# Kernel tuning notes

Hardware: AMD Instinct MI355X
Metric: run time of the kernel (lower is better)

Reference implementation:

```python
import jax, jax.numpy as jnp
import numpy as np

EMBED_DIM = 512
NUM_HEADS = 8
HEAD_DIM = EMBED_DIM // NUM_HEADS  # 64
LN_EPS = 1e-5
SEQ = 2048
BATCH = 2


def sparsemax(z):
    """Sparsemax over last axis: euclidean projection of each row onto the simplex."""
    K = z.shape[-1]
    z_sorted = -jnp.sort(-z, axis=-1)                      # descending
    z_cumsum = jnp.cumsum(z_sorted, axis=-1)
    r = jnp.arange(1, K + 1, dtype=z.dtype)
    support = r * z_sorted > (z_cumsum - 1.0)
    k_int = jnp.sum(support.astype(jnp.int32), axis=-1, keepdims=True)  # support size >= 1
    tau_sum = jnp.take_along_axis(z_cumsum, k_int - 1, axis=-1)
    tau = (tau_sum - 1.0) / k_int.astype(z.dtype)
    return jnp.maximum(z - tau, 0.0)


def layer_norm(x, eps=LN_EPS):
    # per-head pattern normalization over head_dim, no affine (normalize_pattern_affine=False)
    mu = jnp.mean(x, axis=-1, keepdims=True)
    var = jnp.mean(jnp.square(x - mu), axis=-1, keepdims=True)
    return (x - mu) * jax.lax.rsqrt(var + eps)


def setup_inputs() -> dict:
    key = jax.random.key(0)
    ks = jax.random.split(key, 6)
    E = EMBED_DIM
    return {
        "query": jax.random.normal(ks[0], (SEQ, BATCH, E), dtype=jnp.float32),
        "key": jax.random.normal(ks[1], (SEQ, BATCH, E), dtype=jnp.float32),
        "value": jax.random.normal(ks[2], (SEQ, BATCH, E), dtype=jnp.float32),
        "in_proj_weight": 0.02 * jax.random.normal(ks[3], (3 * E, E), dtype=jnp.float32),
        "in_proj_bias": jnp.zeros((3 * E,), dtype=jnp.float32),
        "out_proj_weight": 0.02 * jax.random.normal(ks[4], (E, E), dtype=jnp.float32),
        "out_proj_bias": jnp.zeros((E,), dtype=jnp.float32),
        "update_steps_max": 0,  # single association pass
    }


def reference(query, key, value, in_proj_weight, in_proj_bias,
              out_proj_weight, out_proj_bias, update_steps_max):
    L, B, E = query.shape
    S = key.shape[0]
    H, D = NUM_HEADS, HEAD_DIM
    wq, wk, wv = in_proj_weight[:E], in_proj_weight[E:2 * E], in_proj_weight[2 * E:]
    bq, bk, bv = in_proj_bias[:E], in_proj_bias[E:2 * E], in_proj_bias[2 * E:]
    # projections (torch Linear: x @ W.T + b)
    q = (query @ wq.T + bq).reshape(L, B, H, D)
    k = (key @ wk.T + bk).reshape(S, B, H, D)
    v = (value @ wv.T + bv).reshape(S, B, H, D)
    # pattern normalization (normalize_pattern=True, no affine), then attention scaling
    q = layer_norm(q) * (float(D) ** -0.5)
    k = layer_norm(k)
    v = layer_norm(v)
    # association scores [B, H, Lq, Lk]
    scores = jnp.einsum('ibhd,jbhd->bhij', q, k)
    attn = sparsemax(scores)  # sparse='sparsemax' activation over key axis
    out = jnp.einsum('bhij,jbhd->ibhd', attn, v).reshape(L, B, E)
    return out @ out_proj_weight.T + out_proj_bias
```

## Files before the change

kernel.cpp:

```cpp
#include <hip/hip_runtime.h>

#define SEQ   2048
#define BATCH 2
#define EMB   512
#define NH    8

typedef short bf16x8 __attribute__((ext_vector_type(8)));
typedef float f32x4  __attribute__((ext_vector_type(4)));
typedef unsigned short u16;
typedef unsigned long long u64;

static __device__ __forceinline__ u16 f2bf(float f) {
    unsigned u = __float_as_uint(f);
    return (u16)((u + 0x7FFF + ((u >> 16) & 1)) >> 16);
}
static __device__ __forceinline__ float bf2f(u16 h) {
    return __uint_as_float((unsigned)h << 16);
}
static __device__ __forceinline__ unsigned cvtpk(float a, float b) {
    unsigned r;
    asm("v_cvt_pk_bf16_f32 %0, %1, %2" : "=v"(r) : "v"(a), "v"(b));
    return r;
}
static __device__ __forceinline__ void split8(const float* p, bf16x8& hi, bf16x8& lo) {
    const float4 f0 = *(const float4*)p;
    const float4 f1 = *(const float4*)(p + 4);
    const float fv[8] = {f0.x, f0.y, f0.z, f0.w, f1.x, f1.y, f1.z, f1.w};
    union { unsigned w[4]; bf16x8 v; } H, L;
#pragma unroll
    for (int q = 0; q < 4; ++q) {
        const float a = fv[2 * q], b = fv[2 * q + 1];
        const unsigned h = cvtpk(a, b);
        const float la = a - __uint_as_float(h << 16);
        const float lb = b - __uint_as_float(h & 0xFFFF0000u);
        H.w[q] = h;
        L.w[q] = cvtpk(la, lb);
    }
    hi = H.v; lo = L.v;
}

#define IW4 196608
#define W4  262144
__global__ __launch_bounds__(256) void convert_w(
    const float* __restrict__ ipw, const float* __restrict__ opw,
    u16* __restrict__ iwh, u16* __restrict__ iwl,
    u16* __restrict__ owh, u16* __restrict__ owl)
{
    const int f = blockIdx.x * 256 + threadIdx.x;
    if (f >= W4) return;
    const float* src; u16 *dh, *dl; int o;
    if (f < IW4) { src = ipw; dh = iwh; dl = iwl; o = f; }
    else         { src = opw; dh = owh; dl = owl; o = f - IW4; }
    const float4 x = ((const float4*)src)[o];
    ushort4 hi, lo;
    hi.x = f2bf(x.x); lo.x = f2bf(x.x - bf2f(hi.x));
    hi.y = f2bf(x.y); lo.y = f2bf(x.y - bf2f(hi.y));
    hi.z = f2bf(x.z); lo.z = f2bf(x.z - bf2f(hi.z));
    hi.w = f2bf(x.w); lo.w = f2bf(x.w - bf2f(hi.w));
    ((ushort4*)dh)[o] = hi;
    ((ushort4*)dl)[o] = lo;
}

__global__ __launch_bounds__(256, 4) void gemm_qkv_ln_mfma(
    const float* __restrict__ query, const float* __restrict__ key_in,
    const float* __restrict__ value,
    const u16* __restrict__ iwh, const u16* __restrict__ iwl,
    const float* __restrict__ ipb,
    u16* __restrict__ qhi, u16* __restrict__ qlo,
    u16* __restrict__ khi, u16* __restrict__ klo,
    u16* __restrict__ vth, u16* __restrict__ vtl)
{
    __shared__ float Et[8704];

    const int z = blockIdx.z;
    const float* Xf = (z == 0) ? query : (z == 1) ? key_in : value;
    const float scale = (z == 0) ? 0.125f : 1.0f;

    const int t0  = blockIdx.x * 128;
    const int h   = blockIdx.y;
    const int og0 = z * EMB + h * 64;

    const int tid = threadIdx.x;
    const int w   = tid >> 6;
    const int l   = tid & 63;
    const int c   = l & 15;
    const int g   = l >> 4;

    f32x4 acc[2][4];
#pragma unroll
    for (int mf = 0; mf < 2; ++mf)
#pragma unroll
        for (int nf = 0; nf < 4; ++nf) acc[mf][nf] = (f32x4){0.f, 0.f, 0.f, 0.f};

    const int arow0 = t0 + w * 32 + c;
#pragma unroll
    for (int ks = 0; ks < 16; ++ks) {
        const int k0 = ks * 32 + g * 8;
        bf16x8 ah[2], al[2], bh[4], bl[4];
#pragma unroll
        for (int mf = 0; mf < 2; ++mf)
            split8(&Xf[(size_t)(arow0 + mf * 16) * EMB + k0], ah[mf], al[mf]);
#pragma unroll
        for (int nf = 0; nf < 4; ++nf) {
            const size_t r = (size_t)(og0 + nf * 16 + c) * EMB + k0;
            bh[nf] = *(const bf16x8*)&iwh[r];
            bl[nf] = *(const bf16x8*)&iwl[r];
        }
#pragma unroll
        for (int mf = 0; mf < 2; ++mf)
#pragma unroll
            for (int nf = 0; nf < 4; ++nf) {
                f32x4 t = acc[mf][nf];
                t = __builtin_amdgcn_mfma_f32_16x16x32_bf16(ah[mf], bh[nf], t, 0, 0, 0);
                t = __builtin_amdgcn_mfma_f32_16x16x32_bf16(al[mf], bh[nf], t, 0, 0, 0);
                t = __builtin_amdgcn_mfma_f32_16x16x32_bf16(ah[mf], bl[nf], t, 0, 0, 0);
                acc[mf][nf] = t;
            }
    }

#pragma unroll
    for (int nf = 0; nf < 4; ++nf) {
        const float bj = ipb[og0 + nf * 16 + c];
#pragma unroll
        for (int mf = 0; mf < 2; ++mf)
#pragma unroll
            for (int j = 0; j < 4; ++j) acc[mf][nf][j] += bj;
    }

#pragma unroll
    for (int mf = 0; mf < 2; ++mf) {
        float mu[4], rs[4];
#pragma unroll
        for (int j = 0; j < 4; ++j) {
            float s = acc[mf][0][j] + acc[mf][1][j] + acc[mf][2][j] + acc[mf][3][j];
#pragma unroll
            for (int d = 1; d <= 8; d <<= 1) s += __shfl_xor(s, d);
            mu[j] = s * (1.0f / 64.0f);
        }
#pragma unroll
        for (int j = 0; j < 4; ++j) {
            float t = 0.f;
#pragma unroll
            for (int nf = 0; nf < 4; ++nf) {
                const float dv = acc[mf][nf][j] - mu[j];
                t += dv * dv;
            }
#pragma unroll
            for (int d = 1; d <= 8; d <<= 1) t += __shfl_xor(t, d);
            rs[j] = rsqrtf(t * (1.0f / 64.0f) + 1e-5f) * scale;
        }
#pragma unroll
        for (int j = 0; j < 4; ++j) {
            const int tl = w * 32 + mf * 16 + g * 4 + j;
#pragma unroll
            for (int nf = 0; nf < 4; ++nf) {
                const float val = (acc[mf][nf][j] - mu[j]) * rs[j];
                const int o = nf * 16 + c;
                if (z == 2) Et[o * 133 + tl] = val;
                else        Et[tl * 68 + o]  = val;
            }
        }
    }
    __syncthreads();

    const int part = tid & 7;
    if (z < 2) {
        u16* dh = (z == 0) ? qhi : khi;
        u16* dl = (z == 0) ? qlo : klo;
#pragma unroll
        for (int p = 0; p < 8; ++p) {
            const int seg = p * 32 + (tid >> 3);
            const int tl  = seg & 127;
            const int hl  = seg >> 7;
            const float4 v0 = *(const float4*)&Et[tl * 68 + part * 8];
            const float4 v1 = *(const float4*)&Et[tl * 68 + part * 8 + 4];
            const float vv[8] = {v0.x, v0.y, v0.z, v0.w, v1.x, v1.y, v1.z, v1.w};
            unsigned pk[4];
#pragma unroll
            for (int q = 0; q < 4; ++q) {
                u16 ua, ub;
                if (hl == 0) { ua = f2bf(vv[2*q]); ub = f2bf(vv[2*q+1]); }
                else {
                    const u16 ha = f2bf(vv[2*q]),  hb = f2bf(vv[2*q+1]);
                    ua = f2bf(vv[2*q] - bf2f(ha)); ub = f2bf(vv[2*q+1] - bf2f(hb));
                }
                pk[q] = (unsigned)ua | ((unsigned)ub << 16);
            }
            const int bh_ = (tl & 1) * NH + h;
            const int ii  = (t0 >> 1) + (tl >> 1);
            u16* dst = hl ? dl : dh;
            *(uint4*)&dst[((size_t)bh_ * SEQ + ii) * 64 + part * 8] =
                make_uint4(pk[0], pk[1], pk[2], pk[3]);
        }
    } else {
#pragma unroll
        for (int p = 0; p < 8; ++p) {
            const int seg  = p * 32 + (tid >> 3);
            const int d    = seg & 63;
            const int rest = seg >> 6;
            const int b    = rest & 1;
            const int hl   = rest >> 1;
            float vv[8];
#pragma unroll
            for (int k = 0; k < 8; ++k)
                vv[k] = Et[d * 133 + 2 * (part * 8 + k) + b];
            unsigned pk[4];
#pragma unroll
            for (int q = 0; q < 4; ++q) {
                u16 ua, ub;
                if (hl == 0) { ua = f2bf(vv[2*q]); ub = f2bf(vv[2*q+1]); }
                else {
                    const u16 ha = f2bf(vv[2*q]),  hb = f2bf(vv[2*q+1]);
                    ua = f2bf(vv[2*q] - bf2f(ha)); ub = f2bf(vv[2*q+1] - bf2f(hb));
                }
                pk[q] = (unsigned)ua | ((unsigned)ub << 16);
            }
            const int bh_ = b * NH + h;
            u16* dst = hl ? vtl : vth;
            *(uint4*)&dst[((size_t)bh_ * 64 + d) * SEQ + (t0 >> 1) + part * 8] =
                make_uint4(pk[0], pk[1], pk[2], pk[3]);
        }
    }
}

__global__ __launch_bounds__(512, 2) void attn_sparsemax_mfma(
    const u16* __restrict__ qhi, const u16* __restrict__ qlo,
    const u16* __restrict__ khi, const u16* __restrict__ klo,
    const u16* __restrict__ vth, const u16* __restrict__ vtl,
    u16* __restrict__ aoh, u16* __restrict__ aol)
{
    __shared__ float Opart[8][16][66];
    __shared__ u16   Pst[8][2][16][40];
    __shared__ float wred[2][8][32];
    __shared__ float wcnt[2][8][32];

    const int tid = threadIdx.x;
    const int w   = tid >> 6;
    const int l   = tid & 63;
    const int c   = l & 15;
    const int g   = l >> 4;

    const int wgid = blockIdx.x;
    const int xcd  = wgid & 7;
    const int idx  = wgid >> 3;
    const int bh   = xcd * 2 + (idx >> 6);
    const int q0   = (idx & 63) * 32;

    const size_t bhoff = (size_t)bh * SEQ * 64;
    const u16* qh  = qhi + bhoff;
    const u16* ql  = qlo + bhoff;
    const u16* kh  = khi + bhoff;
    const u16* kl  = klo + bhoff;
    const u16* vh_ = vth + bhoff;
    const u16* vl_ = vtl + bhoff;

    bf16x8 qhf[2][2], qlf[2][2];
#pragma unroll
    for (int nf = 0; nf < 2; ++nf)
#pragma unroll
        for (int kf = 0; kf < 2; ++kf) {
            const size_t a = (size_t)(q0 + nf * 16 + c) * 64 + kf * 32 + g * 8;
            qhf[nf][kf] = *(const bf16x8*)&qh[a];
            qlf[nf][kf] = *(const bf16x8*)&ql[a];
        }

    const int wbase = w * 256;
    f32x4 acc[16][2];
#pragma unroll
    for (int mf = 0; mf < 16; ++mf) {
        const size_t kr = (size_t)(wbase + mf * 16 + c) * 64 + g * 8;
        const bf16x8 kh0 = *(const bf16x8*)&kh[kr];
        const bf16x8 kh1 = *(const bf16x8*)&kh[kr + 32];
        const bf16x8 kl0 = *(const bf16x8*)&kl[kr];
        const bf16x8 kl1 = *(const bf16x8*)&kl[kr + 32];
#pragma unroll
        for (int nf = 0; nf < 2; ++nf) {
            f32x4 t = (f32x4){0.f, 0.f, 0.f, 0.f};
            t = __builtin_amdgcn_mfma_f32_16x16x32_bf16(kh0, qhf[nf][0], t, 0, 0, 0);
            t = __builtin_amdgcn_mfma_f32_16x16x32_bf16(kh1, qhf[nf][1], t, 0, 0, 0);
            t = __builtin_amdgcn_mfma_f32_16x16x32_bf16(kl0, qhf[nf][0], t, 0, 0, 0);
            t = __builtin_amdgcn_mfma_f32_16x16x32_bf16(kl1, qhf[nf][1], t, 0, 0, 0);
            t = __builtin_amdgcn_mfma_f32_16x16x32_bf16(kh0, qlf[nf][0], t, 0, 0, 0);
            t = __builtin_amdgcn_mfma_f32_16x16x32_bf16(kh1, qlf[nf][1], t, 0, 0, 0);
            acc[mf][nf] = t;
        }
    }

    {
        float mx[2];
#pragma unroll
        for (int nf = 0; nf < 2; ++nf) {
            float m = -1e30f;
#pragma unroll
            for (int mf = 0; mf < 16; ++mf)
#pragma unroll
                for (int r = 0; r < 4; ++r) m = fmaxf(m, acc[mf][nf][r]);
            m = fmaxf(m, __shfl_xor(m, 16));
            m = fmaxf(m, __shfl_xor(m, 32));
            mx[nf] = m;
        }
        if (g == 0) { wred[0][w][c] = mx[0]; wred[0][w][16 + c] = mx[1]; }
    }
    __syncthreads();

    float tau[2];
#pragma unroll
    for (int nf = 0; nf < 2; ++nf) {
        float m = -1e30f;
#pragma unroll
        for (int ww = 0; ww < 8; ++ww) m = fmaxf(m, wred[0][ww][nf * 16 + c]);
        tau[nf] = m - 1.0f;
    }

    int cprev[2] = {-1, -1};
    for (int it = 0; it < 24; ++it) {
        const int bs = (~it) & 1;
        float sj[2], cj[2];
#pragma unroll
        for (int nf = 0; nf < 2; ++nf) {
            float s = 0.f, cn = 0.f;
#pragma unroll
            for (int mf = 0; mf < 16; ++mf)
#pragma unroll
                for (int r = 0; r < 4; ++r) {
                    const float v = acc[mf][nf][r];
                    if (v > tau[nf]) { s += v; cn += 1.f; }
                }
            s  += __shfl_xor(s, 16);  cn += __shfl_xor(cn, 16);
            s  += __shfl_xor(s, 32);  cn += __shfl_xor(cn, 32);
            sj[nf] = s; cj[nf] = cn;
        }
        if (g == 0) {
            wred[bs][w][c]      = sj[0];  wred[bs][w][16 + c] = sj[1];
            wcnt[bs][w][c]      = cj[0];  wcnt[bs][w][16 + c] = cj[1];
        }
        __syncthreads();
        int changed = 0;
#pragma unroll
        for (int nf = 0; nf < 2; ++nf) {
            float S = 0.f, C = 0.f;
#pragma unroll
            for (int ww = 0; ww < 8; ++ww) {
                S += wred[bs][ww][nf * 16 + c];
                C += wcnt[bs][ww][nf * 16 + c];
            }
            tau[nf] = (S - 1.0f) / C;
            const int Ci = (int)C;
            changed |= (Ci != cprev[nf]);
            cprev[nf] = Ci;
        }
        if (!__any(changed)) break;
    }

    f32x4 Oacc[4][2];
#pragma unroll
    for (int mo = 0; mo < 4; ++mo)
#pragma unroll
        for (int nf = 0; nf < 2; ++nf) Oacc[mo][nf] = (f32x4){0.f, 0.f, 0.f, 0.f};

#pragma unroll
    for (int ks = 0; ks < 8; ++ks) {
        bf16x8 vh[4], vl[4];
#pragma unroll
        for (int mo = 0; mo < 4; ++mo) {
            const size_t va = (size_t)(mo * 16 + c) * SEQ + wbase + ks * 32 + g * 8;
            vh[mo] = *(const bf16x8*)&vh_[va];
            vl[mo] = *(const bf16x8*)&vl_[va];
        }
#pragma unroll
        for (int nf = 0; nf < 2; ++nf) {
#pragma unroll
            for (int m01 = 0; m01 < 2; ++m01) {
                const f32x4 s = acc[2 * ks + m01][nf];
                const float p0 = fmaxf(s[0] - tau[nf], 0.f);
                const float p1 = fmaxf(s[1] - tau[nf], 0.f);
                const float p2 = fmaxf(s[2] - tau[nf], 0.f);
                const float p3 = fmaxf(s[3] - tau[nf], 0.f);
                const unsigned h0 = cvtpk(p0, p1);
                const unsigned h1 = cvtpk(p2, p3);
                const unsigned l0 = cvtpk(p0 - __uint_as_float(h0 << 16),
                                          p1 - __uint_as_float(h0 & 0xFFFF0000u));
                const unsigned l1 = cvtpk(p2 - __uint_as_float(h1 << 16),
                                          p3 - __uint_as_float(h1 & 0xFFFF0000u));
                *(u64*)&Pst[w][0][c][m01 * 16 + g * 4] = (u64)h0 | ((u64)h1 << 32);
                *(u64*)&Pst[w][1][c][m01 * 16 + g * 4] = (u64)l0 | ((u64)l1 << 32);
            }
            const bf16x8 Bhi = *(const bf16x8*)&Pst[w][0][c][g * 8];
            const bf16x8 Blo = *(const bf16x8*)&Pst[w][1][c][g * 8];
#pragma unroll
            for (int mo = 0; mo < 4; ++mo) {
                f32x4 t = Oacc[mo][nf];
                t = __builtin_amdgcn_mfma_f32_16x16x32_bf16(vh[mo], Bhi, t, 0, 0, 0);
                t = __builtin_amdgcn_mfma_f32_16x16x32_bf16(vh[mo], Blo, t, 0, 0, 0);
                t = __builtin_amdgcn_mfma_f32_16x16x32_bf16(vl[mo], Bhi, t, 0, 0, 0);
                Oacc[mo][nf] = t;
            }
        }
    }

    const int b_ = bh >> 3, h_ = bh & 7;
#pragma unroll
    for (int nf = 0; nf < 2; ++nf) {
        if (nf) __syncthreads();
#pragma unroll
        for (int mo = 0; mo < 4; ++mo)
#pragma unroll
            for (int r = 0; r < 4; ++r)
                Opart[w][c][mo * 16 + 4 * g + r] = Oacc[mo][nf][r];
        __syncthreads();
#pragma unroll
        for (int p = 0; p < 2; ++p) {
            const int idx2 = p * 512 + tid;
            const int d = idx2 & 63;
            const int i = idx2 >> 6;
            float sv = 0.f;
#pragma unroll
            for (int ww = 0; ww < 8; ++ww) sv += Opart[ww][i][d];
            const int irow = q0 + nf * 16 + i;
            const size_t oa = (size_t)(irow * BATCH + b_) * EMB + h_ * 64 + d;
            const u16 hv = f2bf(sv);
            aoh[oa] = hv;
            aol[oa] = f2bf(sv - bf2f(hv));
        }
    }
}

__global__ __launch_bounds__(256, 4) void gemm_out_mfma(
    const u16* __restrict__ aoh, const u16* __restrict__ aol,
    const u16* __restrict__ owh, const u16* __restrict__ owl,
    const float* __restrict__ opb, float* __restrict__ out)
{
    __shared__ float Et[128 * 68];

    const int t0 = blockIdx.x * 128;
    const int o0 = blockIdx.y * 64;

    const int tid = threadIdx.x;
    const int w   = tid >> 6;
    const int l   = tid & 63;
    const int c   = l & 15;
    const int g   = l >> 4;

    f32x4 acc[2][4];
#pragma unroll
    for (int mf = 0; mf < 2; ++mf)
#pragma unroll
        for (int nf = 0; nf < 4; ++nf) acc[mf][nf] = (f32x4){0.f, 0.f, 0.f, 0.f};

    const int arow0 = t0 + w * 32 + c;
#pragma unroll
    for (int ks = 0; ks < 16; ++ks) {
        const int k0 = ks * 32 + g * 8;
        bf16x8 ah[2], al[2], bh[4], bl[4];
#pragma unroll
        for (int mf = 0; mf < 2; ++mf) {
            const size_t r = (size_t)(arow0 + mf * 16) * EMB + k0;
            ah[mf] = *(const bf16x8*)&aoh[r];
            al[mf] = *(const bf16x8*)&aol[r];
        }
#pragma unroll
        for (int nf = 0; nf < 4; ++nf) {
            const size_t r = (size_t)(o0 + nf * 16 + c) * EMB + k0;
            bh[nf] = *(const bf16x8*)&owh[r];
            bl[nf] = *(const bf16x8*)&owl[r];
        }
#pragma unroll
        for (int mf = 0; mf < 2; ++mf)
#pragma unroll
            for (int nf = 0; nf < 4; ++nf) {
                f32x4 t = acc[mf][nf];
                t = __builtin_amdgcn_mfma_f32_16x16x32_bf16(ah[mf], bh[nf], t, 0, 0, 0);
                t = __builtin_amdgcn_mfma_f32_16x16x32_bf16(al[mf], bh[nf], t, 0, 0, 0);
                t = __builtin_amdgcn_mfma_f32_16x16x32_bf16(ah[mf], bl[nf], t, 0, 0, 0);
                acc[mf][nf] = t;
            }
    }

#pragma unroll
    for (int mf = 0; mf < 2; ++mf)
#pragma unroll
        for (int j = 0; j < 4; ++j) {
            const int tl = w * 32 + mf * 16 + g * 4 + j;
#pragma unroll
            for (int nf = 0; nf < 4; ++nf)
                Et[tl * 68 + nf * 16 + c] = acc[mf][nf][j] + opb[o0 + nf * 16 + c];
        }
    __syncthreads();

    const int part = tid & 15;
#pragma unroll
    for (int p = 0; p < 8; ++p) {
        const int row = p * 16 + (tid >> 4);
        const float4 v = *(const float4*)&Et[row * 68 + part * 4];
        *(float4*)&out[(size_t)(t0 + row) * EMB + o0 + part * 4] = v;
    }
}

extern "C" void kernel_launch(void* const* d_in, const int* in_sizes, int n_in,
                              void* d_out, int out_size, void* d_ws, size_t ws_size,
                              hipStream_t stream)
{
    const float* query = (const float*)d_in[0];
    const float* key_  = (const float*)d_in[1];
    const float* value = (const float*)d_in[2];
    const float* ipw   = (const float*)d_in[3];
    const float* ipb   = (const float*)d_in[4];
    const float* opw   = (const float*)d_in[5];
    const float* opb   = (const float*)d_in[6];

    char* ws = (char*)d_ws;
    const size_t MB = 1024 * 1024;
    u16* qhi = (u16*)(ws + 0 * MB);
    u16* qlo = (u16*)(ws + 4 * MB);
    u16* khi = (u16*)(ws + 8 * MB);
    u16* klo = (u16*)(ws + 12 * MB);
    u16* vth = (u16*)(ws + 16 * MB);
    u16* vtl = (u16*)(ws + 20 * MB);
    u16* aoh = (u16*)(ws + 24 * MB);
    u16* aol = (u16*)(ws + 28 * MB);
    u16* iwh = (u16*)(ws + 32 * MB);
    u16* iwl = (u16*)(ws + 34 * MB);
    u16* owh = (u16*)(ws + 36 * MB);
    u16* owl = (u16*)(ws + 37 * MB);
    float* out = (float*)d_out;
    (void)ws_size; (void)in_sizes; (void)n_in; (void)out_size;

    convert_w<<<1024, 256, 0, stream>>>(ipw, opw, iwh, iwl, owh, owl);
    gemm_qkv_ln_mfma<<<dim3(32, 8, 3), 256, 0, stream>>>(
        query, key_, value, iwh, iwl, ipb, qhi, qlo, khi, klo, vth, vtl);
    attn_sparsemax_mfma<<<1024, 512, 0, stream>>>(
        qhi, qlo, khi, klo, vth, vtl, aoh, aol);
    gemm_out_mfma<<<dim3(32, 8), 256, 0, stream>>>(
        aoh, aol, owh, owl, opb, out);
}
```

Before: 369.2 us.

## Halve attention query tile to 16 rows and reduce partial outputs via LDS atomics

The attention kernel now processes 16 query rows per workgroup instead of 32, doubling the grid to 2048 blocks. Per-thread score and output accumulators drop by half, and launch bounds are raised to allow 4 workgroups per CU. The per-wave partial-output buffer and its serial 8-way reduction are replaced by a small zero-initialised LDS tile that waves accumulate into with float atomicAdd. The trade-off is that K and V are reloaded twice as often across the grid and every wave issues atomics into LDS.

New measurement: 492.2 us. 33.3% more time.

```diff
diff --git a/kernel.cpp b/kernel.cpp
--- a/kernel.cpp
+++ b/kernel.cpp
@@ -223,16 +223,16 @@
     }
 }
 
-__global__ __launch_bounds__(512, 2) void attn_sparsemax_mfma(
+__global__ __launch_bounds__(512, 4) void attn_sparsemax_mfma(
     const u16* __restrict__ qhi, const u16* __restrict__ qlo,
     const u16* __restrict__ khi, const u16* __restrict__ klo,
     const u16* __restrict__ vth, const u16* __restrict__ vtl,
     u16* __restrict__ aoh, u16* __restrict__ aol)
 {
-    __shared__ float Opart[8][16][66];
     __shared__ u16   Pst[8][2][16][40];
-    __shared__ float wred[2][8][32];
-    __shared__ float wcnt[2][8][32];
+    __shared__ float O_lds[16][67];
+    __shared__ float wred[2][8][16];
+    __shared__ float wcnt[2][8][16];
 
     const int tid = threadIdx.x;
     const int w   = tid >> 6;
@@ -243,8 +243,10 @@
     const int wgid = blockIdx.x;
     const int xcd  = wgid & 7;
     const int idx  = wgid >> 3;
-    const int bh   = xcd * 2 + (idx >> 6);
-    const int q0   = (idx & 63) * 32;
+    const int bh   = xcd * 2 + (idx >> 7);
+    const int q0   = (idx & 127) * 16;
+
+    for (int f = tid; f < 16 * 67; f += 512) ((float*)O_lds)[f] = 0.f;
 
     const size_t bhoff = (size_t)bh * SEQ * 64;
     const u16* qh  = qhi + bhoff;
@@ -254,18 +256,16 @@
     const u16* vh_ = vth + bhoff;
     const u16* vl_ = vtl + bhoff;
 
-    bf16x8 qhf[2][2], qlf[2][2];
-#pragma unroll
-    for (int nf = 0; nf < 2; ++nf)
-#pragma unroll
-        for (int kf = 0; kf < 2; ++kf) {
-            const size_t a = (size_t)(q0 + nf * 16 + c) * 64 + kf * 32 + g * 8;
-            qhf[nf][kf] = *(const bf16x8*)&qh[a];
-            qlf[nf][kf] = *(const bf16x8*)&ql[a];
-        }
+    bf16x8 qhf[2], qlf[2];
+#pragma unroll
+    for (int kf = 0; kf < 2; ++kf) {
+        const size_t a = (size_t)(q0 + c) * 64 + kf * 32 + g * 8;
+        qhf[kf] = *(const bf16x8*)&qh[a];
+        qlf[kf] = *(const bf16x8*)&ql[a];
+    }
 
     const int wbase = w * 256;
-    f32x4 acc[16][2];
+    f32x4 acc[16];
 #pragma unroll
     for (int mf = 0; mf < 16; ++mf) {
         const size_t kr = (size_t)(wbase + mf * 16 + c) * 64 + g * 8;
@@ -273,155 +273,120 @@
         const bf16x8 kh1 = *(const bf16x8*)&kh[kr + 32];
         const bf16x8 kl0 = *(const bf16x8*)&kl[kr];
         const bf16x8 kl1 = *(const bf16x8*)&kl[kr + 32];
-#pragma unroll
-        for (int nf = 0; nf < 2; ++nf) {
-            f32x4 t = (f32x4){0.f, 0.f, 0.f, 0.f};
-            t = __builtin_amdgcn_mfma_f32_16x16x32_bf16(kh0, qhf[nf][0], t, 0, 0, 0);
-            t = __builtin_amdgcn_mfma_f32_16x16x32_bf16(kh1, qhf[nf][1], t, 0, 0, 0);
-            t = __builtin_amdgcn_mfma_f32_16x16x32_bf16(kl0, qhf[nf][0], t, 0, 0, 0);
-            t = __builtin_amdgcn_mfma_f32_16x16x32_bf16(kl1, qhf[nf][1], t, 0, 0, 0);
-            t = __builtin_amdgcn_mfma_f32_16x16x32_bf16(kh0, qlf[nf][0], t, 0, 0, 0);
-            t = __builtin_amdgcn_mfma_f32_16x16x32_bf16(kh1, qlf[nf][1], t, 0, 0, 0);
-            acc[mf][nf] = t;
-        }
+        f32x4 t = (f32x4){0.f, 0.f, 0.f, 0.f};
+        t = __builtin_amdgcn_mfma_f32_16x16x32_bf16(kh0, qhf[0], t, 0, 0, 0);
+        t = __builtin_amdgcn_mfma_f32_16x16x32_bf16(kh1, qhf[1], t, 0, 0, 0);
+        t = __builtin_amdgcn_mfma_f32_16x16x32_bf16(kl0, qhf[0], t, 0, 0, 0);
+        t = __builtin_amdgcn_mfma_f32_16x16x32_bf16(kl1, qhf[1], t, 0, 0, 0);
+        t = __builtin_amdgcn_mfma_f32_16x16x32_bf16(kh0, qlf[0], t, 0, 0, 0);
+        t = __builtin_amdgcn_mfma_f32_16x16x32_bf16(kh1, qlf[1], t, 0, 0, 0);
+        acc[mf] = t;
     }
 
     {
-        float mx[2];
-#pragma unroll
-        for (int nf = 0; nf < 2; ++nf) {
-            float m = -1e30f;
-#pragma unroll
-            for (int mf = 0; mf < 16; ++mf)
-#pragma unroll
-                for (int r = 0; r < 4; ++r) m = fmaxf(m, acc[mf][nf][r]);
-            m = fmaxf(m, __shfl_xor(m, 16));
-            m = fmaxf(m, __shfl_xor(m, 32));
-            mx[nf] = m;
-        }
-        if (g == 0) { wred[0][w][c] = mx[0]; wred[0][w][16 + c] = mx[1]; }
+        float m = -1e30f;
+#pragma unroll
+        for (int mf = 0; mf < 16; ++mf)
+#pragma unroll
+            for (int r = 0; r < 4; ++r) m = fmaxf(m, acc[mf][r]);
+        m = fmaxf(m, __shfl_xor(m, 16));
+        m = fmaxf(m, __shfl_xor(m, 32));
+        if (g == 0) wred[0][w][c] = m;
     }
     __syncthreads();
 
-    float tau[2];
-#pragma unroll
-    for (int nf = 0; nf < 2; ++nf) {
+    float tau;
+    {
         float m = -1e30f;
 #pragma unroll
-        for (int ww = 0; ww < 8; ++ww) m = fmaxf(m, wred[0][ww][nf * 16 + c]);
-        tau[nf] = m - 1.0f;
-    }
-
-    int cprev[2] = {-1, -1};
+        for (int ww = 0; ww < 8; ++ww) m = fmaxf(m, wred[0][ww][c]);
+        tau = m - 1.0f;
+    }
+
+    int cprev = -1;
     for (int it = 0; it < 24; ++it) {
         const int bs = (~it) & 1;
-        float sj[2], cj[2];
-#pragma unroll
-        for (int nf = 0; nf < 2; ++nf) {
-            float s = 0.f, cn = 0.f;
-#pragma unroll
-            for (int mf = 0; mf < 16; ++mf)
-#pragma unroll
-                for (int r = 0; r < 4; ++r) {
-                    const float v = acc[mf][nf][r];
-                    if (v > tau[nf]) { s += v; cn += 1.f; }
-                }
-            s  += __shfl_xor(s, 16);  cn += __shfl_xor(cn, 16);
-            s  += __shfl_xor(s, 32);  cn += __shfl_xor(cn, 32);
-            sj[nf] = s; cj[nf] = cn;
-        }
-        if (g == 0) {
-            wred[bs][w][c]      = sj[0];  wred[bs][w][16 + c] = sj[1];
-            wcnt[bs][w][c]      = cj[0];  wcnt[bs][w][16 + c] = cj[1];
-        }
+        float s = 0.f, cn = 0.f;
+#pragma unroll
+        for (int mf = 0; mf < 16; ++mf)
+#pragma unroll
+            for (int r = 0; r < 4; ++r) {
+                const float v = acc[mf][r];
+                if (v > tau) { s += v; cn += 1.f; }
+            }
+        s  += __shfl_xor(s, 16);  cn += __shfl_xor(cn, 16);
+        s  += __shfl_xor(s, 32);  cn += __shfl_xor(cn, 32);
+        if (g == 0) { wred[bs][w][c] = s; wcnt[bs][w][c] = cn; }
         __syncthreads();
-        int changed = 0;
-#pragma unroll
-        for (int nf = 0; nf < 2; ++nf) {
-            float S = 0.f, C = 0.f;
-#pragma unroll
-            for (int ww = 0; ww < 8; ++ww) {
-                S += wred[bs][ww][nf * 16 + c];
-                C += wcnt[bs][ww][nf * 16 + c];
-            }
-            tau[nf] = (S - 1.0f) / C;
-            const int Ci = (int)C;
-            changed |= (Ci != cprev[nf]);
-            cprev[nf] = Ci;
-        }
+        float S = 0.f, C = 0.f;
+#pragma unroll
+        for (int ww = 0; ww < 8; ++ww) {
+            S += wred[bs][ww][c];
+            C += wcnt[bs][ww][c];
+        }
+        tau = (S - 1.0f) / C;
+        const int Ci = (int)C;
+        const int changed = (Ci != cprev);
+        cprev = Ci;
         if (!__any(changed)) break;
     }
 
-    f32x4 Oacc[4][2];
-#pragma unroll
-    for (int mo = 0; mo < 4; ++mo)
-#pragma unroll
-        for (int nf = 0; nf < 2; ++nf) Oacc[mo][nf] = (f32x4){0.f, 0.f, 0.f, 0.f};
+    f32x4 Oacc[4];
+#pragma unroll
+    for (int mo = 0; mo < 4; ++mo) Oacc[mo] = (f32x4){0.f, 0.f, 0.f, 0.f};
 
 #pragma unroll
     for (int ks = 0; ks < 8; ++ks) {
-        bf16x8 vh[4], vl[4];
+#pragma unroll
+        for (int m01 = 0; m01 < 2; ++m01) {
+            const f32x4 s = acc[2 * ks + m01];
+            const float p0 = fmaxf(s[0] - tau, 0.f);
+            const float p1 = fmaxf(s[1] - tau, 0.f);
+            const float p2 = fmaxf(s[2] - tau, 0.f);
+            const float p3 = fmaxf(s[3] - tau, 0.f);
+            const unsigned h0 = cvtpk(p0, p1);
+            const unsigned h1 = cvtpk(p2, p3);
+            const unsigned l0 = cvtpk(p0 - __uint_as_float(h0 << 16),
+                                      p1 - __uint_as_float(h0 & 0xFFFF0000u));
+            const unsigned l1 = cvtpk(p2 - __uint_as_float(h1 << 16),
+                                      p3 - __uint_as_float(h1 & 0xFFFF0000u));
+            *(u64*)&Pst[w][0][c][m01 * 16 + g * 4] = (u64)h0 | ((u64)h1 << 32);
+            *(u64*)&Pst[w][1][c][m01 * 16 + g * 4] = (u64)l0 | ((u64)l1 << 32);
+        }
+        const bf16x8 Bhi = *(const bf16x8*)&Pst[w][0][c][g * 8];
+        const bf16x8 Blo = *(const bf16x8*)&Pst[w][1][c][g * 8];
 #pragma unroll
         for (int mo = 0; mo < 4; ++mo) {
             const size_t va = (size_t)(mo * 16 + c) * SEQ + wbase + ks * 32 + g * 8;
-            vh[mo] = *(const bf16x8*)&vh_[va];
-            vl[mo] = *(const bf16x8*)&vl_[va];
-        }
-#pragma unroll
-        for (int nf = 0; nf < 2; ++nf) {
-#pragma unroll
-            for (int m01 = 0; m01 < 2; ++m01) {
-                const f32x4 s = acc[2 * ks + m01][nf];
-                const float p0 = fmaxf(s[0] - tau[nf], 0.f);
-                const float p1 = fmaxf(s[1] - tau[nf], 0.f);
-                const float p2 = fmaxf(s[2] - tau[nf], 0.f);
-                const float p3 = fmaxf(s[3] - tau[nf], 0.f);
-                const unsigned h0 = cvtpk(p0, p1);
-                const unsigned h1 = cvtpk(p2, p3);
-                const unsigned l0 = cvtpk(p0 - __uint_as_float(h0 << 16),
-                                          p1 - __uint_as_float(h0 & 0xFFFF0000u));
-                const unsigned l1 = cvtpk(p2 - __uint_as_float(h1 << 16),
-                                          p3 - __uint_as_float(h1 & 0xFFFF0000u));
-                *(u64*)&Pst[w][0][c][m01 * 16 + g * 4] = (u64)h0 | ((u64)h1 << 32);
-                *(u64*)&Pst[w][1][c][m01 * 16 + g * 4] = (u64)l0 | ((u64)l1 << 32);
-            }
-            const bf16x8 Bhi = *(const bf16x8*)&Pst[w][0][c][g * 8];
-            const bf16x8 Blo = *(const bf16x8*)&Pst[w][1][c][g * 8];
-#pragma unroll
-            for (int mo = 0; mo < 4; ++mo) {
-                f32x4 t = Oacc[mo][nf];
-                t = __builtin_amdgcn_mfma_f32_16x16x32_bf16(vh[mo], Bhi, t, 0, 0, 0);
-                t = __builtin_amdgcn_mfma_f32_16x16x32_bf16(vh[mo], Blo, t, 0, 0, 0);
-                t = __builtin_amdgcn_mfma_f32_16x16x32_bf16(vl[mo], Bhi, t, 0, 0, 0);
-                Oacc[mo][nf] = t;
-            }
-        }
-    }
+            const bf16x8 vh = *(const bf16x8*)&vh_[va];
+            const bf16x8 vl = *(const bf16x8*)&vl_[va];
+            f32x4 t = Oacc[mo];
+            t = __builtin_amdgcn_mfma_f32_16x16x32_bf16(vh, Bhi, t, 0, 0, 0);
+            t = __builtin_amdgcn_mfma_f32_16x16x32_bf16(vh, Blo, t, 0, 0, 0);
+            t = __builtin_amdgcn_mfma_f32_16x16x32_bf16(vl, Bhi, t, 0, 0, 0);
+            Oacc[mo] = t;
+        }
+    }
+
+#pragma unroll
+    for (int mo = 0; mo < 4; ++mo)
+#pragma unroll
+        for (int r = 0; r < 4; ++r)
+            atomicAdd(&O_lds[c][mo * 16 + g * 4 + r], Oacc[mo][r]);
+    __syncthreads();
 
     const int b_ = bh >> 3, h_ = bh & 7;
 #pragma unroll
-    for (int nf = 0; nf < 2; ++nf) {
-        if (nf) __syncthreads();
-#pragma unroll
-        for (int mo = 0; mo < 4; ++mo)
-#pragma unroll
-            for (int r = 0; r < 4; ++r)
-                Opart[w][c][mo * 16 + 4 * g + r] = Oacc[mo][nf][r];
-        __syncthreads();
-#pragma unroll
-        for (int p = 0; p < 2; ++p) {
-            const int idx2 = p * 512 + tid;
-            const int d = idx2 & 63;
-            const int i = idx2 >> 6;
-            float sv = 0.f;
-#pragma unroll
-            for (int ww = 0; ww < 8; ++ww) sv += Opart[ww][i][d];
-            const int irow = q0 + nf * 16 + i;
-            const size_t oa = (size_t)(irow * BATCH + b_) * EMB + h_ * 64 + d;
-            const u16 hv = f2bf(sv);
-            aoh[oa] = hv;
-            aol[oa] = f2bf(sv - bf2f(hv));
-        }
+    for (int p = 0; p < 2; ++p) {
+        const int idx2 = p * 512 + tid;
+        const int d = idx2 & 63;
+        const int i = idx2 >> 6;
+        const float sv = O_lds[i][d];
+        const int irow = q0 + i;
+        const size_t oa = (size_t)(irow * BATCH + b_) * EMB + h_ * 64 + d;
+        const u16 hv = f2bf(sv);
+        aoh[oa] = hv;
+        aol[oa] = f2bf(sv - bf2f(hv));
     }
 }
 
@@ -528,7 +493,7 @@
     convert_w<<<1024, 256, 0, stream>>>(ipw, opw, iwh, iwl, owh, owl);
     gemm_qkv_ln_mfma<<<dim3(32, 8, 3), 256, 0, stream>>>(
         query, key_, value, iwh, iwl, ipb, qhi, qlo, khi, klo, vth, vtl);
-    attn_sparsemax_mfma<<<1024, 512, 0, stream>>>(
+    attn_sparsemax_mfma<<<2048, 512, 0, stream>>>(
         qhi, qlo, khi, klo, vth, vtl, aoh, aol);
     gemm_out_mfma<<<dim3(32, 8), 256, 0, stream>>>(
         aoh, aol, owh, owl, opb, out);
```

## Compact sparsemax candidates into LDS lists and drop weight pre-conversion kernel

Applied to the files above, without the earlier changes.

The sparsemax threshold search now first collects, per query row, the scores above max-1 into a shared-memory candidate list (capacity 160). Each wave then iterates the tau fixed point over that short list with wave-level shuffles, avoiding the block-wide barrier per iteration over all 2048 scores. If any row overflows the list, the old full iteration runs instead. The separate weight hi/lo conversion kernel is also removed: both GEMMs now split the fp32 weights inline. The per-wave output reduction is replaced by LDS float atomics into a single tile. Costs are LDS atomic contention and redundant per-block weight splitting.

New measurement: 445.1 us. +20.6%, slower.

```diff
diff --git a/kernel.cpp b/kernel.cpp
--- a/kernel.cpp
+++ b/kernel.cpp
@@ -4,6 +4,7 @@
 #define BATCH 2
 #define EMB   512
 #define NH    8
+#define CAP   160
 
 typedef short bf16x8 __attribute__((ext_vector_type(8)));
 typedef float f32x4  __attribute__((ext_vector_type(4)));
@@ -39,33 +40,10 @@
     hi = H.v; lo = L.v;
 }
 
-#define IW4 196608
-#define W4  262144
-__global__ __launch_bounds__(256) void convert_w(
-    const float* __restrict__ ipw, const float* __restrict__ opw,
-    u16* __restrict__ iwh, u16* __restrict__ iwl,
-    u16* __restrict__ owh, u16* __restrict__ owl)
-{
-    const int f = blockIdx.x * 256 + threadIdx.x;
-    if (f >= W4) return;
-    const float* src; u16 *dh, *dl; int o;
-    if (f < IW4) { src = ipw; dh = iwh; dl = iwl; o = f; }
-    else         { src = opw; dh = owh; dl = owl; o = f - IW4; }
-    const float4 x = ((const float4*)src)[o];
-    ushort4 hi, lo;
-    hi.x = f2bf(x.x); lo.x = f2bf(x.x - bf2f(hi.x));
-    hi.y = f2bf(x.y); lo.y = f2bf(x.y - bf2f(hi.y));
-    hi.z = f2bf(x.z); lo.z = f2bf(x.z - bf2f(hi.z));
-    hi.w = f2bf(x.w); lo.w = f2bf(x.w - bf2f(hi.w));
-    ((ushort4*)dh)[o] = hi;
-    ((ushort4*)dl)[o] = lo;
-}
-
 __global__ __launch_bounds__(256, 4) void gemm_qkv_ln_mfma(
     const float* __restrict__ query, const float* __restrict__ key_in,
     const float* __restrict__ value,
-    const u16* __restrict__ iwh, const u16* __restrict__ iwl,
-    const float* __restrict__ ipb,
+    const float* __restrict__ ipw, const float* __restrict__ ipb,
     u16* __restrict__ qhi, u16* __restrict__ qlo,
     u16* __restrict__ khi, u16* __restrict__ klo,
     u16* __restrict__ vth, u16* __restrict__ vtl)
@@ -101,11 +79,8 @@
         for (int mf = 0; mf < 2; ++mf)
             split8(&Xf[(size_t)(arow0 + mf * 16) * EMB + k0], ah[mf], al[mf]);
 #pragma unroll
-        for (int nf = 0; nf < 4; ++nf) {
-            const size_t r = (size_t)(og0 + nf * 16 + c) * EMB + k0;
-            bh[nf] = *(const bf16x8*)&iwh[r];
-            bl[nf] = *(const bf16x8*)&iwl[r];
-        }
+        for (int nf = 0; nf < 4; ++nf)
+            split8(&ipw[(size_t)(og0 + nf * 16 + c) * EMB + k0], bh[nf], bl[nf]);
 #pragma unroll
         for (int mf = 0; mf < 2; ++mf)
 #pragma unroll
@@ -229,10 +204,14 @@
     const u16* __restrict__ vth, const u16* __restrict__ vtl,
     u16* __restrict__ aoh, u16* __restrict__ aol)
 {
-    __shared__ float Opart[8][16][66];
     __shared__ u16   Pst[8][2][16][40];
+    __shared__ float O_lds[32][67];
+    __shared__ float clist[32][CAP];
+    __shared__ int   ccnt[32];
+    __shared__ float taus[32];
     __shared__ float wred[2][8][32];
-    __shared__ float wcnt[2][8][32];
+    __shared__ float wcnt_s[2][8][32];
+    __shared__ int   oflow;
 
     const int tid = threadIdx.x;
     const int w   = tid >> 6;
@@ -245,6 +224,10 @@
     const int idx  = wgid >> 3;
     const int bh   = xcd * 2 + (idx >> 6);
     const int q0   = (idx & 63) * 32;
+
+    for (int f = tid; f < 32 * 67; f += 512) ((float*)O_lds)[f] = 0.f;
+    if (tid < 32) ccnt[tid] = 0;
+    if (tid == 0) oflow = 0;
 
     const size_t bhoff = (size_t)bh * SEQ * 64;
     const u16* qh  = qhi + bhoff;
@@ -303,53 +286,112 @@
     }
     __syncthreads();
 
-    float tau[2];
+    float tau0[2];
 #pragma unroll
     for (int nf = 0; nf < 2; ++nf) {
         float m = -1e30f;
 #pragma unroll
         for (int ww = 0; ww < 8; ++ww) m = fmaxf(m, wred[0][ww][nf * 16 + c]);
-        tau[nf] = m - 1.0f;
-    }
-
-    int cprev[2] = {-1, -1};
-    for (int it = 0; it < 24; ++it) {
-        const int bs = (~it) & 1;
-        float sj[2], cj[2];
-#pragma unroll
-        for (int nf = 0; nf < 2; ++nf) {
-            float s = 0.f, cn = 0.f;
-#pragma unroll
-            for (int mf = 0; mf < 16; ++mf)
-#pragma unroll
-                for (int r = 0; r < 4; ++r) {
-                    const float v = acc[mf][nf][r];
-                    if (v > tau[nf]) { s += v; cn += 1.f; }
+        tau0[nf] = m - 1.0f;
+    }
+
+#pragma unroll
+    for (int nf = 0; nf < 2; ++nf) {
+        const int row = nf * 16 + c;
+#pragma unroll
+        for (int mf = 0; mf < 16; ++mf)
+#pragma unroll
+            for (int r = 0; r < 4; ++r) {
+                const float v = acc[mf][nf][r];
+                if (v > tau0[nf]) {
+                    const int pos = atomicAdd(&ccnt[row], 1);
+                    if (pos < CAP) clist[row][pos] = v;
+                    else           oflow = 1;
                 }
-            s  += __shfl_xor(s, 16);  cn += __shfl_xor(cn, 16);
-            s  += __shfl_xor(s, 32);  cn += __shfl_xor(cn, 32);
-            sj[nf] = s; cj[nf] = cn;
-        }
-        if (g == 0) {
-            wred[bs][w][c]      = sj[0];  wred[bs][w][16 + c] = sj[1];
-            wcnt[bs][w][c]      = cj[0];  wcnt[bs][w][16 + c] = cj[1];
+            }
+    }
+    __syncthreads();
+
+    float tau[2];
+    if (oflow) {
+        tau[0] = tau0[0]; tau[1] = tau0[1];
+        int cprev[2] = {-1, -1};
+        for (int it = 0; it < 24; ++it) {
+            const int bs = (~it) & 1;
+            float sj[2], cj[2];
+#pragma unroll
+            for (int nf = 0; nf < 2; ++nf) {
+                float s = 0.f, cn = 0.f;
+#pragma unroll
+                for (int mf = 0; mf < 16; ++mf)
+#pragma unroll
+                    for (int r = 0; r < 4; ++r) {
+                        const float v = acc[mf][nf][r];
+                        if (v > tau[nf]) { s += v; cn += 1.f; }
+                    }
+                s  += __shfl_xor(s, 16);  cn += __shfl_xor(cn, 16);
+                s  += __shfl_xor(s, 32);  cn += __shfl_xor(cn, 32);
+                sj[nf] = s; cj[nf] = cn;
+            }
+            if (g == 0) {
+#pragma unroll
+                for (int nf = 0; nf < 2; ++nf) {
+                    wred[bs][w][nf * 16 + c]  = sj[nf];
+                    wcnt_s[bs][w][nf * 16 + c] = cj[nf];
+                }
+            }
+            __syncthreads();
+            int changed = 0;
+#pragma unroll
+            for (int nf = 0; nf < 2; ++nf) {
+                float S = 0.f, C = 0.f;
+#pragma unroll
+                for (int ww = 0; ww < 8; ++ww) {
+                    S += wred[bs][ww][nf * 16 + c];
+                    C += wcnt_s[bs][ww][nf * 16 + c];
+                }
+                tau[nf] = (S - 1.0f) / C;
+                const int Ci = (int)C;
+                changed |= (Ci != cprev[nf]);
+                cprev[nf] = Ci;
+            }
+            if (!__any(changed)) break;
+        }
+    } else {
+#pragma unroll 1
+        for (int rr = 0; rr < 4; ++rr) {
+            const int i = w * 4 + rr;
+            const int n = ccnt[i];
+            float t0r = -1e30f;
+#pragma unroll
+            for (int ww = 0; ww < 8; ++ww) t0r = fmaxf(t0r, wred[0][ww][i]);
+            t0r -= 1.0f;
+            const float v0 = (l       < n) ? clist[i][l]       : -1e30f;
+            const float v1 = (l + 64  < n) ? clist[i][l + 64]  : -1e30f;
+            const float v2 = (l + 128 < n) ? clist[i][l + 128] : -1e30f;
+            float tw = t0r;
+            int cp = -1;
+#pragma unroll 1
+            for (int it = 0; it < 24; ++it) {
+                float s = 0.f, cn = 0.f;
+                if (v0 > tw) { s += v0; cn += 1.f; }
+                if (v1 > tw) { s += v1; cn += 1.f; }
+                if (v2 > tw) { s += v2; cn += 1.f; }
+#pragma unroll
+                for (int d = 1; d <= 32; d <<= 1) {
+                    s  += __shfl_xor(s, d);
+                    cn += __shfl_xor(cn, d);
+                }
+                tw = (s - 1.0f) / cn;
+                const int ci = (int)cn;
+                if (ci == cp) break;
+                cp = ci;
+            }
+            if (l == 0) taus[i] = tw;
         }
         __syncthreads();
-        int changed = 0;
-#pragma unroll
-        for (int nf = 0; nf < 2; ++nf) {
-            float S = 0.f, C = 0.f;
-#pragma unroll
-            for (int ww = 0; ww < 8; ++ww) {
-                S += wred[bs][ww][nf * 16 + c];
-                C += wcnt[bs][ww][nf * 16 + c];
-            }
-            tau[nf] = (S - 1.0f) / C;
-            const int Ci = (int)C;
-            changed |= (Ci != cprev[nf]);
-            cprev[nf] = Ci;
-        }
-        if (!__any(changed)) break;
+        tau[0] = taus[c];
+        tau[1] = taus[16 + c];
     }
 
     f32x4 Oacc[4][2];
@@ -398,37 +440,34 @@
         }
     }
 
+#pragma unroll
+    for (int nf = 0; nf < 2; ++nf)
+#pragma unroll
+        for (int mo = 0; mo < 4; ++mo)
+#pragma unroll
+            for (int r = 0; r < 4; ++r)
+                atomicAdd(&O_lds[nf * 16 + c][mo * 16 + g * 4 + r], Oacc[mo][nf][r]);
+    __syncthreads();
+
     const int b_ = bh >> 3, h_ = bh & 7;
 #pragma unroll
-    for (int nf = 0; nf < 2; ++nf) {
-        if (nf) __syncthreads();
-#pragma unroll
-        for (int mo = 0; mo < 4; ++mo)
-#pragma unroll
-            for (int r = 0; r < 4; ++r)
-                Opart[w][c][mo * 16 + 4 * g + r] = Oacc[mo][nf][r];
-        __syncthreads();
-#pragma unroll
-        for (int p = 0; p < 2; ++p) {
-            const int idx2 = p * 512 + tid;
-            const int d = idx2 & 63;
-            const int i = idx2 >> 6;
-            float sv = 0.f;
-#pragma unroll
-            for (int ww = 0; ww < 8; ++ww) sv += Opart[ww][i][d];
-            const int irow = q0 + nf * 16 + i;
-            const size_t oa = (size_t)(irow * BATCH + b_) * EMB + h_ * 64 + d;
-            const u16 hv = f2bf(sv);
-            aoh[oa] = hv;
-            aol[oa] = f2bf(sv - bf2f(hv));
-        }
+    for (int p = 0; p < 4; ++p) {
+        const int idx2 = p * 512 + tid;
+        const int d = idx2 & 63;
+        const int i = idx2 >> 6;
+        const float sv = O_lds[i][d];
+        const int irow = q0 + i;
+        const size_t oa = (size_t)(irow * BATCH + b_) * EMB + h_ * 64 + d;
+        const u16 hv = f2bf(sv);
+        aoh[oa] = hv;
+        aol[oa] = f2bf(sv - bf2f(hv));
     }
 }
 
 __global__ __launch_bounds__(256, 4) void gemm_out_mfma(
     const u16* __restrict__ aoh, const u16* __restrict__ aol,
-    const u16* __restrict__ owh, const u16* __restrict__ owl,
-    const float* __restrict__ opb, float* __restrict__ out)
+    const float* __restrict__ opw, const float* __restrict__ opb,
+    float* __restrict__ out)
 {
     __shared__ float Et[128 * 68];
 
@@ -459,11 +498,8 @@
             al[mf] = *(const bf16x8*)&aol[r];
         }
 #pragma unroll
-        for (int nf = 0; nf < 4; ++nf) {
-            const size_t r = (size_t)(o0 + nf * 16 + c) * EMB + k0;
-            bh[nf] = *(const bf16x8*)&owh[r];
-            bl[nf] = *(const bf16x8*)&owl[r];
-        }
+        for (int nf = 0; nf < 4; ++nf)
+            split8(&opw[(size_t)(o0 + nf * 16 + c) * EMB + k0], bh[nf], bl[nf]);
 #pragma unroll
         for (int mf = 0; mf < 2; ++mf)
 #pragma unroll
@@ -518,18 +554,13 @@
     u16* vtl = (u16*)(ws + 20 * MB);
     u16* aoh = (u16*)(ws + 24 * MB);
     u16* aol = (u16*)(ws + 28 * MB);
-    u16* iwh = (u16*)(ws + 32 * MB);
-    u16* iwl = (u16*)(ws + 34 * MB);
-    u16* owh = (u16*)(ws + 36 * MB);
-    u16* owl = (u16*)(ws + 37 * MB);
     float* out = (float*)d_out;
     (void)ws_size; (void)in_sizes; (void)n_in; (void)out_size;
 
-    convert_w<<<1024, 256, 0, stream>>>(ipw, opw, iwh, iwl, owh, owl);
     gemm_qkv_ln_mfma<<<dim3(32, 8, 3), 256, 0, stream>>>(
-        query, key_, value, iwh, iwl, ipb, qhi, qlo, khi, klo, vth, vtl);
+        query, key_, value, ipw, ipb, qhi, qlo, khi, klo, vth, vtl);
     attn_sparsemax_mfma<<<1024, 512, 0, stream>>>(
         qhi, qlo, khi, klo, vth, vtl, aoh, aol);
     gemm_out_mfma<<<dim3(32, 8), 256, 0, stream>>>(
-        aoh, aol, owh, owl, opb, out);
-}
+        aoh, aol, opw, opb, out);
+}
```
